# Performance work log

Hardware: AMD Instinct MI355X
Metric: run time of the kernel (lower is better)

Reference implementation:

```python
import jax, jax.numpy as jnp
import numpy as np

ALPHABET = 26
VGENES = 60
JGENES = 20
E = 1024      # embedding_dim (= 2*VJ + LATENT)
H = 2048      # hidden_dim
LATENT = 768  # latent_space_dim
VJ = 128      # embedding_dim_VJ
L = 4096      # sequence length
X_IDX = 23    # all_letters.index('X')
B_IDX = 1     # all_letters.index('B')


def setup_inputs() -> dict:
    key = jax.random.key(0)
    ks = jax.random.split(key, 16)
    s = lambda fan_in: 1.0 / np.sqrt(fan_in)
    u = lambda k, shape, sc: jax.random.uniform(k, shape, jnp.float32, -sc, sc)
    return {
        "x": jax.random.randint(ks[0], (L,), 0, ALPHABET, dtype=jnp.int32),
        "Vg": jax.random.randint(ks[1], (1,), 0, VGENES, dtype=jnp.int32),
        "Jg": jax.random.randint(ks[2], (1,), 0, JGENES, dtype=jnp.int32),
        "tick": 0,
        "emb": jax.random.normal(ks[3], (ALPHABET, E), jnp.float32),
        "embV": jax.random.normal(ks[4], (VGENES, VJ), jnp.float32),
        "embJ": jax.random.normal(ks[5], (JGENES, VJ), jnp.float32),
        "W_ih_enc": u(ks[6], (4 * H, E), s(H)),
        "W_hh_enc": u(ks[7], (4 * H, H), s(H)),
        "b_ih_enc": u(ks[8], (4 * H,), s(H)),
        "b_hh_enc": u(ks[9], (4 * H,), s(H)),
        "W_ls": u(ks[10], (LATENT, H), s(H)),
        "b_ls": u(ks[11], (LATENT,), s(H)),
        "W_ih_dec": u(ks[12], (4 * E, E), s(E)),
        "W_hh_dec": u(ks[13], (4 * E, E), s(E)),
        "b_ih_dec": u(ks[14], (4 * E,), s(E)),
        "b_hh_dec": u(ks[15], (4 * E,), s(E)),
    }


def _lstm_cell(x_t, h, c, W_ih, W_hh, b):
    # torch gate order: i, f, g, o
    g = x_t @ W_ih.T + h @ W_hh.T + b
    i, f, gg, o = jnp.split(g, 4, axis=-1)
    c = jax.nn.sigmoid(f) * c + jax.nn.sigmoid(i) * jnp.tanh(gg)
    h = jax.nn.sigmoid(o) * jnp.tanh(c)
    return h, c


def reference(x, Vg, Jg, tick, emb, embV, embJ,
              W_ih_enc, W_hh_enc, b_ih_enc, b_hh_enc,
              W_ls, b_ls,
              W_ih_dec, W_hh_dec, b_ih_dec, b_hh_dec):
    # ---- encode ----
    embedded = emb[x]                       # [L, E]
    b_enc = b_ih_enc + b_hh_enc

    def enc_step(carry, x_t):
        h, c = carry
        h, c = _lstm_cell(x_t, h, c, W_ih_enc, W_hh_enc, b_enc)
        return (h, c), None

    h0 = jnp.zeros((H,), embedded.dtype)
    (h_n, _), _ = jax.lax.scan(enc_step, (h0, h0), embedded)
    latent = jnp.tanh(h_n @ W_ls.T + b_ls)  # [LATENT]

    # ---- concat latent with V/J gene embeddings -> [E] ----
    latent_cat = jnp.concatenate([embV[Vg[0]], latent, embJ[Jg[0]]])

    # ---- decode: feed own output back as next input ----
    b_dec = b_ih_dec + b_hh_dec
    prev0 = emb[X_IDX]                      # start letter embedding [E]

    def dec_step(carry, _):
        prev, h, c = carry
        h, c = _lstm_cell(prev, h, c, W_ih_dec, W_hh_dec, b_dec)
        return (h, h, c), h

    (_, _, _), outs = jax.lax.scan(dec_step, (prev0, latent_cat, latent_cat),
                                   None, length=L - 2)  # [L-2, E]

    seq = jnp.concatenate([prev0[None], outs, emb[B_IDX][None]], axis=0)  # [L, E]
    recon = seq[::-1][:, None, :]           # [L, 1, E] (original reverses the list)

    return latent_cat[None, None, :], recon, embedded
```

## Files before the change

kernel.cpp:

```cpp
#include <hip/hip_runtime.h>
#include <hip/hip_bf16.h>
#include <stdint.h>

#define NWG 256
typedef unsigned long long u64;

typedef __attribute__((ext_vector_type(8))) short bf16x8;
typedef __attribute__((ext_vector_type(4))) float f32x4;

__device__ __forceinline__ short f2bf(float f) {
    unsigned u = __float_as_uint(f);
    unsigned r = (u + 0x7fffu + ((u >> 16) & 1u)) >> 16;
    return (short)r;
}

__device__ __forceinline__ void gload16(const void* g, void* l) {
    __builtin_amdgcn_global_load_lds(
        (const __attribute__((address_space(1))) void*)g,
        (__attribute__((address_space(3))) void*)l, 16, 0, 0);
}

__device__ __forceinline__ u64 ald(const u64* p) {
    return __hip_atomic_load(p, __ATOMIC_RELAXED, __HIP_MEMORY_SCOPE_AGENT);
}
__device__ __forceinline__ void ast(u64* p, u64 v) {
    __hip_atomic_store(p, v, __ATOMIC_RELAXED, __HIP_MEMORY_SCOPE_AGENT);
}
__device__ __forceinline__ u64 pack(unsigned tag, float f) {
    return ((u64)tag << 32) | (u64)(unsigned)__float_as_uint(f);
}

__global__ void prep_all(const int* __restrict__ x, const int* __restrict__ Vg, const int* __restrict__ Jg,
                         const float* __restrict__ emb, const float* __restrict__ embV, const float* __restrict__ embJ,
                         const float* __restrict__ Wih_e,
                         const float* __restrict__ Wih_d, const float* __restrict__ Whh_d,
                         float* __restrict__ out,
                         short* __restrict__ Abf, short* __restrict__ Wbf,
                         float* __restrict__ wsum,
                         u64* __restrict__ bufE, u64* __restrict__ bufD)
{
    const size_t i0 = (size_t)blockIdx.x * blockDim.x + threadIdx.x;
    const size_t str = (size_t)gridDim.x * blockDim.x;
    for (size_t i = i0; i < (size_t)4096 * 1024; i += str) {
        int t = (int)(i >> 10), j = (int)(i & 1023);
        float v = emb[(size_t)x[t] * 1024 + j];
        out[4195328 + i] = v;
        Abf[i] = f2bf(v);
    }
    for (size_t i = i0; i < (size_t)8192 * 1024; i += str) Wbf[i] = f2bf(Wih_e[i]);
    for (size_t i = i0; i < (size_t)4096 * 1024; i += str) wsum[i] = Wih_d[i] + Whh_d[i];
    for (size_t i = i0; i < 1024; i += str) {
        out[1024 + i] = emb[1 * 1024 + i];
        out[1024 + (size_t)4095 * 1024 + i] = emb[23 * 1024 + i];
    }
    for (size_t i = i0; i < 6144; i += str) bufE[i] = 0ull;
    for (size_t i = i0; i < 3072; i += str) {
        u64 v = 0ull;
        if (i < 1024) {
            if (i < 128)      v = pack(0u, embV[(size_t)Vg[0] * 128 + i]);
            else if (i < 896) v = 0xFFFFFFFF00000000ull;
            else              v = pack(0u, embJ[(size_t)Jg[0] * 128 + (i - 896)]);
        }
        bufD[i] = v;
    }
    for (size_t i = i0; i < 128; i += str) {
        out[i]       = embV[(size_t)Vg[0] * 128 + i];
        out[896 + i] = embJ[(size_t)Jg[0] * 128 + i];
    }
}

__global__ void prep_pg(const float* __restrict__ Wih_d, const float* __restrict__ emb,
                        const float* __restrict__ bih_d, const float* __restrict__ bhh_d,
                        float* __restrict__ pg)
{
    const int lane = threadIdx.x & 63, wv = threadIdx.x >> 6;
    const float* prev0 = emb + 23 * 1024;
    for (int rr = 0; rr < 16; rr++) {
        int row = blockIdx.x * 64 + wv * 16 + rr;
        float s = 0.f;
        #pragma unroll
        for (int q = 0; q < 16; q++) {
            int k = lane + q * 64;
            s += Wih_d[(size_t)row * 1024 + k] * prev0[k];
        }
        for (int o = 32; o; o >>= 1) s += __shfl_xor(s, o, 64);
        if (lane == 0) pg[row] = s + bih_d[row] + bhh_d[row];
    }
}

__launch_bounds__(256, 2)
__global__ void gemm_xgates(const short* __restrict__ A,
                            const short* __restrict__ B,
                            const float* __restrict__ bih, const float* __restrict__ bhh,
                            float* __restrict__ C)
{
    __shared__ short lA[128 * 32];
    __shared__ short lB[128 * 32];
    const int bid = blockIdx.x;
    const int mb = bid >> 6;
    const int nb = bid & 63;
    const int tid = threadIdx.x, lane = tid & 63, wv = tid >> 6;
    const int wr = wv >> 1, wc = wv & 1;
    const int Mbase = mb * 128, Nbase = nb * 128;
    f32x4 acc[4][4] = {};

    for (int kt = 0; kt < 32; kt++) {
        __syncthreads();
        const int k0b = kt * 64;
        #pragma unroll
        for (int c = 0; c < 2; c++) {
            int f = tid * 16 + c * 4096;
            int row = f >> 6, kb = f & 63;
            const char* ga = (const char*)A + (size_t)(Mbase + row) * 2048 + k0b + kb;
            const char* gb = (const char*)B + (size_t)(Nbase + row) * 2048 + k0b + kb;
            gload16(ga, (char*)lA + wv * 1024 + c * 4096);
            gload16(gb, (char*)lB + wv * 1024 + c * 4096);
        }
        asm volatile("s_waitcnt vmcnt(0)" ::: "memory");
        __syncthreads();
        bf16x8 af[4], bf[4];
        #pragma unroll
        for (int i = 0; i < 4; i++) {
            af[i] = *(const bf16x8*)&lA[(wr * 64 + i * 16 + (lane & 15)) * 32 + (lane >> 4) * 8];
            bf[i] = *(const bf16x8*)&lB[(wc * 64 + i * 16 + (lane & 15)) * 32 + (lane >> 4) * 8];
        }
        #pragma unroll
        for (int i = 0; i < 4; i++)
            #pragma unroll
            for (int j = 0; j < 4; j++)
                acc[i][j] = __builtin_amdgcn_mfma_f32_16x16x32_bf16(af[i], bf[j], acc[i][j], 0, 0, 0);
    }
    #pragma unroll
    for (int i = 0; i < 4; i++) {
        #pragma unroll
        for (int j = 0; j < 4; j++) {
            int col = Nbase + wc * 64 + j * 16 + (lane & 15);
            float bv = bih[col] + bhh[col];
            #pragma unroll
            for (int r = 0; r < 4; r++) {
                int row = Mbase + wr * 64 + i * 16 + (lane >> 4) * 4 + r;
                C[(size_t)row * 8192 + col] = acc[i][j][r] + bv;
            }
        }
    }
}

__launch_bounds__(512, 2)
__global__ void rnn_seq(const float* __restrict__ Whh_e,
                        const float* __restrict__ Wls,
                        const float* __restrict__ bls,
                        const float* __restrict__ Whh_d,
                        const float* __restrict__ Gx,
                        const float* __restrict__ wsum,
                        const float* __restrict__ bih_d, const float* __restrict__ bhh_d,
                        const float* __restrict__ pg,
                        u64* __restrict__ bufE,
                        u64* __restrict__ bufD,
                        float* __restrict__ out)
{
    const int w = blockIdx.x;
    const int tid = threadIdx.x;
    const int lane = tid & 63, wv = tid >> 6;
    __shared__ float hl[2048];
    __shared__ float red[32];
    __shared__ float cst[8];

    float we[128];
    #pragma unroll
    for (int rr = 0; rr < 4; rr++) {
        int ridx = wv * 4 + rr;
        const float* src = Whh_e + (size_t)((ridx >> 3) * 2048 + 8 * w + (ridx & 7)) * 2048 + lane;
        #pragma unroll
        for (int j = 0; j < 32; j++) we[rr * 32 + j] = src[64 * j];
    }
    if (tid < 8) cst[tid] = 0.f;
    const int grow = (tid >> 3) * 2048 + 8 * w + (tid & 7);
    __syncthreads();

    #pragma unroll 1
    for (int t = 0; t < 4096; t++) {
        float gxv = 0.f;
        if (tid < 32) gxv = Gx[(size_t)t * 8192 + grow];

        const unsigned tg = (unsigned)t;
        const u64* src = bufE + (size_t)(t % 3) * 2048 + wv * 256 + lane;
        u64 v0, v1, v2, v3;
        for (;;) {
            v0 = ald(src); v1 = ald(src + 64); v2 = ald(src + 128); v3 = ald(src + 192);
            bool ok = ((unsigned)(v0 >> 32) == tg) & ((unsigned)(v1 >> 32) == tg)
                    & ((unsigned)(v2 >> 32) == tg) & ((unsigned)(v3 >> 32) == tg);
            if (__all(ok)) break;
        }
        int b = wv * 256 + lane;
        hl[b]       = __uint_as_float((unsigned)v0);
        hl[b + 64]  = __uint_as_float((unsigned)v1);
        hl[b + 128] = __uint_as_float((unsigned)v2);
        hl[b + 192] = __uint_as_float((unsigned)v3);
        __syncthreads();

        float a0 = 0.f, a1 = 0.f, a2 = 0.f, a3 = 0.f;
        #pragma unroll
        for (int j = 0; j < 32; j++) {
            float hv = hl[lane + 64 * j];
            a0 += we[j] * hv; a1 += we[32 + j] * hv;
            a2 += we[64 + j] * hv; a3 += we[96 + j] * hv;
        }
        #pragma unroll
        for (int o = 32; o; o >>= 1) {
            a0 += __shfl_xor(a0, o, 64); a1 += __shfl_xor(a1, o, 64);
            a2 += __shfl_xor(a2, o, 64); a3 += __shfl_xor(a3, o, 64);
        }
        if (lane == 0) {
            red[wv * 4]     = a0; red[wv * 4 + 1] = a1;
            red[wv * 4 + 2] = a2; red[wv * 4 + 3] = a3;
        }
        __syncthreads();

        if (tid < 32) {
            float g = red[tid] + gxv;
            float gi = __shfl(g, (tid & 7), 64);
            float gf = __shfl(g, (tid & 7) + 8, 64);
            float gg = __shfl(g, (tid & 7) + 16, 64);
            float go = __shfl(g, (tid & 7) + 24, 64);
            if (tid < 8) {
                float c  = cst[tid];
                float ig = 1.f / (1.f + expf(-gi));
                float fg = 1.f / (1.f + expf(-gf));
                float og = 1.f / (1.f + expf(-go));
                float cn = fg * c + ig * tanhf(gg);
                float hn = og * tanhf(cn);
                cst[tid] = cn;
                ast(&bufE[(size_t)((t + 1) % 3) * 2048 + 8 * w + tid], pack((unsigned)(t + 1), hn));
            }
        }
        __syncthreads();
    }

    {
        const unsigned tg = 4096u;
        const u64* src = bufE + (size_t)2048 + wv * 256 + lane;
        u64 v0, v1, v2, v3;
        for (;;) {
            v0 = ald(src); v1 = ald(src + 64); v2 = ald(src + 128); v3 = ald(src + 192);
            bool ok = ((unsigned)(v0 >> 32) == tg) & ((unsigned)(v1 >> 32) == tg)
                    & ((unsigned)(v2 >> 32) == tg) & ((unsigned)(v3 >> 32) == tg);
            if (__all(ok)) break;
        }
        int b = wv * 256 + lane;
        hl[b]       = __uint_as_float((unsigned)v0);
        hl[b + 64]  = __uint_as_float((unsigned)v1);
        hl[b + 128] = __uint_as_float((unsigned)v2);
        hl[b + 192] = __uint_as_float((unsigned)v3);
        __syncthreads();

        if (wv < 3) {
            int row = 3 * w + wv;
            const float* wr = Wls + (size_t)row * 2048 + lane;
            float s = 0.f;
            #pragma unroll
            for (int q = 0; q < 32; q++) s += wr[64 * q] * hl[lane + 64 * q];
            for (int o = 32; o; o >>= 1) s += __shfl_xor(s, o, 64);
            if (lane == 0) {
                float lv = tanhf(s + bls[row]);
                out[128 + row] = lv;
                ast(&bufD[128 + row], pack(0u, lv));
            }
        }
        __syncthreads();
    }

    float wd[32];
    #pragma unroll
    for (int rr = 0; rr < 2; rr++) {
        int ridx = wv * 2 + rr;
        const float* src = wsum + (size_t)((ridx >> 2) * 1024 + 4 * w + (ridx & 3)) * 1024 + lane;
        #pragma unroll
        for (int j = 0; j < 16; j++) wd[rr * 16 + j] = src[64 * j];
    }
    float bdv = 0.f, pgv = 0.f;
    if (tid < 16) {
        int R = (tid >> 2) * 1024 + 4 * w + (tid & 3);
        bdv = bih_d[R] + bhh_d[R];
        pgv = pg[R];
    }
    if (tid < 4) {
        const u64* p = bufD + 4 * w + tid;
        u64 v;
        do { v = ald(p); } while ((unsigned)(v >> 32) != 0u);
        cst[tid] = __uint_as_float((unsigned)v);
    }
    __syncthreads();

    #pragma unroll 1
    for (int s = 1; s <= 4094; s++) {
        const unsigned tg = (unsigned)(s - 1);
        const u64* src = bufD + (size_t)((s - 1) % 3) * 1024 + wv * 128 + lane;
        u64 v0, v1;
        for (;;) {
            v0 = ald(src); v1 = ald(src + 64);
            bool ok = ((unsigned)(v0 >> 32) == tg) & ((unsigned)(v1 >> 32) == tg);
            if (__all(ok)) break;
        }
        hl[wv * 128 + lane]      = __uint_as_float((unsigned)v0);
        hl[wv * 128 + lane + 64] = __uint_as_float((unsigned)v1);
        __syncthreads();

        float a0 = 0.f, a1 = 0.f;
        if (s == 1) {
            #pragma unroll
            for (int rr = 0; rr < 2; rr++) {
                int ridx = wv * 2 + rr;
                const float* srcw = Whh_d + (size_t)((ridx >> 2) * 1024 + 4 * w + (ridx & 3)) * 1024 + lane;
                float a = 0.f;
                #pragma unroll
                for (int j = 0; j < 16; j++) a += srcw[64 * j] * hl[lane + 64 * j];
                if (rr) a1 = a; else a0 = a;
            }
        } else {
            #pragma unroll
            for (int j = 0; j < 16; j++) {
                float hv = hl[lane + 64 * j];
                a0 += wd[j] * hv; a1 += wd[16 + j] * hv;
            }
        }
        #pragma unroll
        for (int o = 32; o; o >>= 1) {
            a0 += __shfl_xor(a0, o, 64); a1 += __shfl_xor(a1, o, 64);
        }
        if (lane == 0) { red[wv * 2] = a0; red[wv * 2 + 1] = a1; }
        __syncthreads();

        if (tid < 16) {
            float g = red[tid] + ((s == 1) ? pgv : bdv);
            float gi = __shfl(g, (tid & 3), 64);
            float gf = __shfl(g, (tid & 3) + 4, 64);
            float gg = __shfl(g, (tid & 3) + 8, 64);
            float go = __shfl(g, (tid & 3) + 12, 64);
            if (tid < 4) {
                float c  = cst[tid];
                float ig = 1.f / (1.f + expf(-gi));
                float fg = 1.f / (1.f + expf(-gf));
                float og = 1.f / (1.f + expf(-go));
                float cn = fg * c + ig * tanhf(gg);
                float hn = og * tanhf(cn);
                cst[tid] = cn;
                out[1024 + (size_t)(4095 - s) * 1024 + 4 * w + tid] = hn;
                ast(&bufD[(size_t)(s % 3) * 1024 + 4 * w + tid], pack((unsigned)s, hn));
            }
        }
        __syncthreads();
    }
}

extern "C" void kernel_launch(void* const* d_in, const int* in_sizes, int n_in,
                              void* d_out, int out_size, void* d_ws, size_t ws_size,
                              hipStream_t stream)
{
    const int* x      = (const int*)d_in[0];
    const int* Vg     = (const int*)d_in[1];
    const int* Jg     = (const int*)d_in[2];
    const float* emb   = (const float*)d_in[4];
    const float* embV  = (const float*)d_in[5];
    const float* embJ  = (const float*)d_in[6];
    const float* Wih_e = (const float*)d_in[7];
    const float* Whh_e = (const float*)d_in[8];
    const float* bih_e = (const float*)d_in[9];
    const float* bhh_e = (const float*)d_in[10];
    const float* Wls   = (const float*)d_in[11];
    const float* bls   = (const float*)d_in[12];
    const float* Wih_d = (const float*)d_in[13];
    const float* Whh_d = (const float*)d_in[14];
    const float* bih_d = (const float*)d_in[15];
    const float* bhh_d = (const float*)d_in[16];
    float* out = (float*)d_out;

    char* ws = (char*)d_ws;
    u64*   bufE = (u64*)ws;
    u64*   bufD = (u64*)(ws + 49152);
    float* pg   = (float*)(ws + 73728);
    short* Abf  = (short*)(ws + 90368);
    short* Wbf  = (short*)(ws + 8478976);
    float* wsum = (float*)(ws + 25256192);
    float* Gx   = (float*)(ws + 42033408);

    prep_all<<<1024, 256, 0, stream>>>(x, Vg, Jg, emb, embV, embJ,
                                       Wih_e, Wih_d, Whh_d,
                                       out, Abf, Wbf, wsum, bufE, bufD);
    prep_pg<<<64, 256, 0, stream>>>(Wih_d, emb, bih_d, bhh_d, pg);
    gemm_xgates<<<2048, 256, 0, stream>>>(Abf, Wbf, bih_e, bhh_e, Gx);

    void* args[] = { (void*)&Whh_e, (void*)&Wls, (void*)&bls, (void*)&Whh_d,
                     (void*)&Gx, (void*)&wsum, (void*)&bih_d, (void*)&bhh_d, (void*)&pg,
                     (void*)&bufE, (void*)&bufD, (void*)&out };
    hipLaunchCooperativeKernel((const void*)rnn_seq, dim3(NWG), dim3(512), args, 0, stream);
}
```

Measured before the change: 20.93 ms.

## Give each wave one hidden unit's four gates and remove per-step block barriers

```diff
diff --git a/kernel.cpp b/kernel.cpp
--- a/kernel.cpp
+++ b/kernel.cpp
@@ -136,10 +136,11 @@
         for (int j = 0; j < 4; j++) {
             int col = Nbase + wc * 64 + j * 16 + (lane & 15);
             float bv = bih[col] + bhh[col];
+            int dst = ((col & 2047) << 2) | (col >> 11);
             #pragma unroll
             for (int r = 0; r < 4; r++) {
                 int row = Mbase + wr * 64 + i * 16 + (lane >> 4) * 4 + r;
-                C[(size_t)row * 8192 + col] = acc[i][j][r] + bv;
+                C[(size_t)row * 8192 + dst] = acc[i][j][r] + bv;
             }
         }
     }
@@ -150,7 +151,7 @@
                         const float* __restrict__ Wls,
                         const float* __restrict__ bls,
                         const float* __restrict__ Whh_d,
-                        const float* __restrict__ Gx,
+                        const float* __restrict__ Gxt,
                         const float* __restrict__ wsum,
                         const float* __restrict__ bih_d, const float* __restrict__ bhh_d,
                         const float* __restrict__ pg,
@@ -161,104 +162,89 @@
     const int w = blockIdx.x;
     const int tid = threadIdx.x;
     const int lane = tid & 63, wv = tid >> 6;
-    __shared__ float hl[2048];
-    __shared__ float red[32];
-    __shared__ float cst[8];
-
-    float we[128];
+    __shared__ float hl[2][2048];
+
+    const int hidxE = 8 * w + wv;
+    float4 we[4][8];
     #pragma unroll
-    for (int rr = 0; rr < 4; rr++) {
-        int ridx = wv * 4 + rr;
-        const float* src = Whh_e + (size_t)((ridx >> 3) * 2048 + 8 * w + (ridx & 7)) * 2048 + lane;
-        #pragma unroll
-        for (int j = 0; j < 32; j++) we[rr * 32 + j] = src[64 * j];
-    }
-    if (tid < 8) cst[tid] = 0.f;
-    const int grow = (tid >> 3) * 2048 + 8 * w + (tid & 7);
-    __syncthreads();
+    for (int g = 0; g < 4; g++) {
+        const float* src = Whh_e + (size_t)(g * 2048 + hidxE) * 2048 + 4 * lane;
+        #pragma unroll
+        for (int jj = 0; jj < 8; jj++) we[g][jj] = *(const float4*)(src + 256 * jj);
+    }
+    float c = 0.f;
+
+    float gx = 0.f;
+    if (lane < 4) gx = Gxt[(size_t)hidxE * 4 + lane];
 
     #pragma unroll 1
     for (int t = 0; t < 4096; t++) {
-        float gxv = 0.f;
-        if (tid < 32) gxv = Gx[(size_t)t * 8192 + grow];
-
         const unsigned tg = (unsigned)t;
-        const u64* src = bufE + (size_t)(t % 3) * 2048 + wv * 256 + lane;
-        u64 v0, v1, v2, v3;
+        const u64* p = bufE + (size_t)(t % 3) * 2048 + wv * 256 + 4 * lane;
+        u64 a0 = ald(p), a1 = ald(p + 1), a2 = ald(p + 2), a3 = ald(p + 3);
         for (;;) {
-            v0 = ald(src); v1 = ald(src + 64); v2 = ald(src + 128); v3 = ald(src + 192);
-            bool ok = ((unsigned)(v0 >> 32) == tg) & ((unsigned)(v1 >> 32) == tg)
-                    & ((unsigned)(v2 >> 32) == tg) & ((unsigned)(v3 >> 32) == tg);
-            if (__all(ok)) break;
-        }
-        int b = wv * 256 + lane;
-        hl[b]       = __uint_as_float((unsigned)v0);
-        hl[b + 64]  = __uint_as_float((unsigned)v1);
-        hl[b + 128] = __uint_as_float((unsigned)v2);
-        hl[b + 192] = __uint_as_float((unsigned)v3);
-        __syncthreads();
-
-        float a0 = 0.f, a1 = 0.f, a2 = 0.f, a3 = 0.f;
-        #pragma unroll
-        for (int j = 0; j < 32; j++) {
-            float hv = hl[lane + 64 * j];
-            a0 += we[j] * hv; a1 += we[32 + j] * hv;
-            a2 += we[64 + j] * hv; a3 += we[96 + j] * hv;
+            bool ok = ((unsigned)(a0 >> 32) == tg) & ((unsigned)(a1 >> 32) == tg)
+                    & ((unsigned)(a2 >> 32) == tg) & ((unsigned)(a3 >> 32) == tg);
+            if (__builtin_expect(__all(ok), 1)) break;
+            a0 = ald(p); a1 = ald(p + 1); a2 = ald(p + 2); a3 = ald(p + 3);
+        }
+        float4 hv = { __uint_as_float((unsigned)a0), __uint_as_float((unsigned)a1),
+                      __uint_as_float((unsigned)a2), __uint_as_float((unsigned)a3) };
+        *(float4*)&hl[t & 1][wv * 256 + 4 * lane] = hv;
+        __syncthreads();
+
+        float gx_next = 0.f;
+        if (lane < 4 && t < 4095) gx_next = Gxt[(size_t)(t + 1) * 8192 + hidxE * 4 + lane];
+
+        float s0 = 0.f, s1 = 0.f, s2 = 0.f, s3 = 0.f;
+        const float4* hp = (const float4*)hl[t & 1];
+        #pragma unroll
+        for (int jj = 0; jj < 8; jj++) {
+            float4 h4 = hp[lane + 64 * jj];
+            s0 += we[0][jj].x * h4.x; s0 += we[0][jj].y * h4.y; s0 += we[0][jj].z * h4.z; s0 += we[0][jj].w * h4.w;
+            s1 += we[1][jj].x * h4.x; s1 += we[1][jj].y * h4.y; s1 += we[1][jj].z * h4.z; s1 += we[1][jj].w * h4.w;
+            s2 += we[2][jj].x * h4.x; s2 += we[2][jj].y * h4.y; s2 += we[2][jj].z * h4.z; s2 += we[2][jj].w * h4.w;
+            s3 += we[3][jj].x * h4.x; s3 += we[3][jj].y * h4.y; s3 += we[3][jj].z * h4.z; s3 += we[3][jj].w * h4.w;
         }
         #pragma unroll
         for (int o = 32; o; o >>= 1) {
-            a0 += __shfl_xor(a0, o, 64); a1 += __shfl_xor(a1, o, 64);
-            a2 += __shfl_xor(a2, o, 64); a3 += __shfl_xor(a3, o, 64);
-        }
-        if (lane == 0) {
-            red[wv * 4]     = a0; red[wv * 4 + 1] = a1;
-            red[wv * 4 + 2] = a2; red[wv * 4 + 3] = a3;
-        }
-        __syncthreads();
-
-        if (tid < 32) {
-            float g = red[tid] + gxv;
-            float gi = __shfl(g, (tid & 7), 64);
-            float gf = __shfl(g, (tid & 7) + 8, 64);
-            float gg = __shfl(g, (tid & 7) + 16, 64);
-            float go = __shfl(g, (tid & 7) + 24, 64);
-            if (tid < 8) {
-                float c  = cst[tid];
-                float ig = 1.f / (1.f + expf(-gi));
-                float fg = 1.f / (1.f + expf(-gf));
-                float og = 1.f / (1.f + expf(-go));
-                float cn = fg * c + ig * tanhf(gg);
-                float hn = og * tanhf(cn);
-                cst[tid] = cn;
-                ast(&bufE[(size_t)((t + 1) % 3) * 2048 + 8 * w + tid], pack((unsigned)(t + 1), hn));
-            }
-        }
-        __syncthreads();
+            s0 += __shfl_xor(s0, o, 64); s1 += __shfl_xor(s1, o, 64);
+            s2 += __shfl_xor(s2, o, 64); s3 += __shfl_xor(s3, o, 64);
+        }
+        float gi = s0 + __shfl(gx, 0, 64);
+        float gf = s1 + __shfl(gx, 1, 64);
+        float gg = s2 + __shfl(gx, 2, 64);
+        float go = s3 + __shfl(gx, 3, 64);
+        float ig = 1.f / (1.f + expf(-gi));
+        float fg = 1.f / (1.f + expf(-gf));
+        float og = 1.f / (1.f + expf(-go));
+        c = fg * c + ig * tanhf(gg);
+        float hn = og * tanhf(c);
+        if (lane == 0) ast(&bufE[(size_t)((t + 1) % 3) * 2048 + hidxE], pack(tg + 1, hn));
+        gx = gx_next;
     }
 
     {
         const unsigned tg = 4096u;
-        const u64* src = bufE + (size_t)2048 + wv * 256 + lane;
-        u64 v0, v1, v2, v3;
+        const u64* p = bufE + (size_t)2048 + wv * 256 + 4 * lane;
+        u64 a0 = ald(p), a1 = ald(p + 1), a2 = ald(p + 2), a3 = ald(p + 3);
         for (;;) {
-            v0 = ald(src); v1 = ald(src + 64); v2 = ald(src + 128); v3 = ald(src + 192);
-            bool ok = ((unsigned)(v0 >> 32) == tg) & ((unsigned)(v1 >> 32) == tg)
-                    & ((unsigned)(v2 >> 32) == tg) & ((unsigned)(v3 >> 32) == tg);
-            if (__all(ok)) break;
-        }
-        int b = wv * 256 + lane;
-        hl[b]       = __uint_as_float((unsigned)v0);
-        hl[b + 64]  = __uint_as_float((unsigned)v1);
-        hl[b + 128] = __uint_as_float((unsigned)v2);
-        hl[b + 192] = __uint_as_float((unsigned)v3);
+            bool ok = ((unsigned)(a0 >> 32) == tg) & ((unsigned)(a1 >> 32) == tg)
+                    & ((unsigned)(a2 >> 32) == tg) & ((unsigned)(a3 >> 32) == tg);
+            if (__builtin_expect(__all(ok), 1)) break;
+            a0 = ald(p); a1 = ald(p + 1); a2 = ald(p + 2); a3 = ald(p + 3);
+        }
+        float4 hv = { __uint_as_float((unsigned)a0), __uint_as_float((unsigned)a1),
+                      __uint_as_float((unsigned)a2), __uint_as_float((unsigned)a3) };
+        *(float4*)&hl[0][wv * 256 + 4 * lane] = hv;
         __syncthreads();
 
         if (wv < 3) {
             int row = 3 * w + wv;
-            const float* wr = Wls + (size_t)row * 2048 + lane;
+            const float* wr = Wls + (size_t)row * 2048;
             float s = 0.f;
             #pragma unroll
-            for (int q = 0; q < 32; q++) s += wr[64 * q] * hl[lane + 64 * q];
+            for (int q = 0; q < 32; q++) s += wr[lane + 64 * q] * hl[0][lane + 64 * q];
             for (int o = 32; o; o >>= 1) s += __shfl_xor(s, o, 64);
             if (lane == 0) {
                 float lv = tanhf(s + bls[row]);
@@ -269,86 +255,87 @@
         __syncthreads();
     }
 
-    float wd[32];
-    #pragma unroll
-    for (int rr = 0; rr < 2; rr++) {
-        int ridx = wv * 2 + rr;
-        const float* src = wsum + (size_t)((ridx >> 2) * 1024 + 4 * w + (ridx & 3)) * 1024 + lane;
-        #pragma unroll
-        for (int j = 0; j < 16; j++) wd[rr * 16 + j] = src[64 * j];
-    }
-    float bdv = 0.f, pgv = 0.f;
-    if (tid < 16) {
-        int R = (tid >> 2) * 1024 + 4 * w + (tid & 3);
-        bdv = bih_d[R] + bhh_d[R];
-        pgv = pg[R];
-    }
-    if (tid < 4) {
-        const u64* p = bufD + 4 * w + tid;
+    const int hidxD = 4 * w + (wv & 3);
+    float4 wd[4][4];
+    float bdv = 0.f, pgv = 0.f, cD = 0.f;
+    if (wv < 4) {
+        #pragma unroll
+        for (int g = 0; g < 4; g++) {
+            const float* src = wsum + (size_t)(g * 1024 + hidxD) * 1024 + 4 * lane;
+            #pragma unroll
+            for (int jj = 0; jj < 4; jj++) wd[g][jj] = *(const float4*)(src + 256 * jj);
+        }
+        if (lane < 4) {
+            int R = lane * 1024 + hidxD;
+            bdv = bih_d[R] + bhh_d[R];
+            pgv = pg[R];
+        }
+        const u64* pc = bufD + hidxD;
         u64 v;
-        do { v = ald(p); } while ((unsigned)(v >> 32) != 0u);
-        cst[tid] = __uint_as_float((unsigned)v);
-    }
-    __syncthreads();
+        do { v = ald(pc); } while ((unsigned)(v >> 32) != 0u);
+        cD = __uint_as_float((unsigned)v);
+    }
 
     #pragma unroll 1
     for (int s = 1; s <= 4094; s++) {
         const unsigned tg = (unsigned)(s - 1);
-        const u64* src = bufD + (size_t)((s - 1) % 3) * 1024 + wv * 128 + lane;
-        u64 v0, v1;
+        const u64* p = bufD + (size_t)((s - 1) % 3) * 1024 + wv * 128 + 2 * lane;
+        u64 a0 = ald(p), a1 = ald(p + 1);
         for (;;) {
-            v0 = ald(src); v1 = ald(src + 64);
-            bool ok = ((unsigned)(v0 >> 32) == tg) & ((unsigned)(v1 >> 32) == tg);
-            if (__all(ok)) break;
-        }
-        hl[wv * 128 + lane]      = __uint_as_float((unsigned)v0);
-        hl[wv * 128 + lane + 64] = __uint_as_float((unsigned)v1);
-        __syncthreads();
-
-        float a0 = 0.f, a1 = 0.f;
-        if (s == 1) {
-            #pragma unroll
-            for (int rr = 0; rr < 2; rr++) {
-                int ridx = wv * 2 + rr;
-                const float* srcw = Whh_d + (size_t)((ridx >> 2) * 1024 + 4 * w + (ridx & 3)) * 1024 + lane;
-                float a = 0.f;
+            bool ok = ((unsigned)(a0 >> 32) == tg) & ((unsigned)(a1 >> 32) == tg);
+            if (__builtin_expect(__all(ok), 1)) break;
+            a0 = ald(p); a1 = ald(p + 1);
+        }
+        float2 hv = { __uint_as_float((unsigned)a0), __uint_as_float((unsigned)a1) };
+        *(float2*)&hl[(s - 1) & 1][wv * 128 + 2 * lane] = hv;
+        __syncthreads();
+
+        if (wv < 4) {
+            float s0 = 0.f, s1 = 0.f, s2 = 0.f, s3 = 0.f;
+            const float4* hp = (const float4*)hl[(s - 1) & 1];
+            if (s == 1) {
                 #pragma unroll
-                for (int j = 0; j < 16; j++) a += srcw[64 * j] * hl[lane + 64 * j];
-                if (rr) a1 = a; else a0 = a;
-            }
-        } else {
-            #pragma unroll
-            for (int j = 0; j < 16; j++) {
-                float hv = hl[lane + 64 * j];
-                a0 += wd[j] * hv; a1 += wd[16 + j] * hv;
-            }
-        }
-        #pragma unroll
-        for (int o = 32; o; o >>= 1) {
-            a0 += __shfl_xor(a0, o, 64); a1 += __shfl_xor(a1, o, 64);
-        }
-        if (lane == 0) { red[wv * 2] = a0; red[wv * 2 + 1] = a1; }
-        __syncthreads();
-
-        if (tid < 16) {
-            float g = red[tid] + ((s == 1) ? pgv : bdv);
-            float gi = __shfl(g, (tid & 3), 64);
-            float gf = __shfl(g, (tid & 3) + 4, 64);
-            float gg = __shfl(g, (tid & 3) + 8, 64);
-            float go = __shfl(g, (tid & 3) + 12, 64);
-            if (tid < 4) {
-                float c  = cst[tid];
-                float ig = 1.f / (1.f + expf(-gi));
-                float fg = 1.f / (1.f + expf(-gf));
-                float og = 1.f / (1.f + expf(-go));
-                float cn = fg * c + ig * tanhf(gg);
-                float hn = og * tanhf(cn);
-                cst[tid] = cn;
-                out[1024 + (size_t)(4095 - s) * 1024 + 4 * w + tid] = hn;
-                ast(&bufD[(size_t)(s % 3) * 1024 + 4 * w + tid], pack((unsigned)s, hn));
-            }
-        }
-        __syncthreads();
+                for (int g = 0; g < 4; g++) {
+                    const float* srcw = Whh_d + (size_t)(g * 1024 + hidxD) * 1024 + 4 * lane;
+                    float a = 0.f;
+                    #pragma unroll
+                    for (int jj = 0; jj < 4; jj++) {
+                        float4 w4 = *(const float4*)(srcw + 256 * jj);
+                        float4 h4 = hp[lane + 64 * jj];
+                        a += w4.x * h4.x + w4.y * h4.y + w4.z * h4.z + w4.w * h4.w;
+                    }
+                    if (g == 0) s0 = a; else if (g == 1) s1 = a; else if (g == 2) s2 = a; else s3 = a;
+                }
+            } else {
+                #pragma unroll
+                for (int jj = 0; jj < 4; jj++) {
+                    float4 h4 = hp[lane + 64 * jj];
+                    s0 += wd[0][jj].x * h4.x; s0 += wd[0][jj].y * h4.y; s0 += wd[0][jj].z * h4.z; s0 += wd[0][jj].w * h4.w;
+                    s1 += wd[1][jj].x * h4.x; s1 += wd[1][jj].y * h4.y; s1 += wd[1][jj].z * h4.z; s1 += wd[1][jj].w * h4.w;
+                    s2 += wd[2][jj].x * h4.x; s2 += wd[2][jj].y * h4.y; s2 += wd[2][jj].z * h4.z; s2 += wd[2][jj].w * h4.w;
+                    s3 += wd[3][jj].x * h4.x; s3 += wd[3][jj].y * h4.y; s3 += wd[3][jj].z * h4.z; s3 += wd[3][jj].w * h4.w;
+                }
+            }
+            #pragma unroll
+            for (int o = 32; o; o >>= 1) {
+                s0 += __shfl_xor(s0, o, 64); s1 += __shfl_xor(s1, o, 64);
+                s2 += __shfl_xor(s2, o, 64); s3 += __shfl_xor(s3, o, 64);
+            }
+            float bb = (s == 1) ? pgv : bdv;
+            float gi = s0 + __shfl(bb, 0, 64);
+            float gf = s1 + __shfl(bb, 1, 64);
+            float gg = s2 + __shfl(bb, 2, 64);
+            float go = s3 + __shfl(bb, 3, 64);
+            float ig = 1.f / (1.f + expf(-gi));
+            float fg = 1.f / (1.f + expf(-gf));
+            float og = 1.f / (1.f + expf(-go));
+            cD = fg * cD + ig * tanhf(gg);
+            float hn = og * tanhf(cD);
+            if (lane == 0) {
+                out[1024 + (size_t)(4095 - s) * 1024 + hidxD] = hn;
+                ast(&bufD[(size_t)(s % 3) * 1024 + hidxD], pack((unsigned)s, hn));
+            }
+        }
     }
 }
 
@@ -381,16 +368,16 @@
     short* Abf  = (short*)(ws + 90368);
     short* Wbf  = (short*)(ws + 8478976);
     float* wsum = (float*)(ws + 25256192);
-    float* Gx   = (float*)(ws + 42033408);
+    float* Gxt  = (float*)(ws + 42033408);
 
     prep_all<<<1024, 256, 0, stream>>>(x, Vg, Jg, emb, embV, embJ,
                                        Wih_e, Wih_d, Whh_d,
                                        out, Abf, Wbf, wsum, bufE, bufD);
     prep_pg<<<64, 256, 0, stream>>>(Wih_d, emb, bih_d, bhh_d, pg);
-    gemm_xgates<<<2048, 256, 0, stream>>>(Abf, Wbf, bih_e, bhh_e, Gx);
+    gemm_xgates<<<2048, 256, 0, stream>>>(Abf, Wbf, bih_e, bhh_e, Gxt);
 
     void* args[] = { (void*)&Whh_e, (void*)&Wls, (void*)&bls, (void*)&Whh_d,
-                     (void*)&Gx, (void*)&wsum, (void*)&bih_d, (void*)&bhh_d, (void*)&pg,
+                     (void*)&Gxt, (void*)&wsum, (void*)&bih_d, (void*)&bhh_d, (void*)&pg,
                      (void*)&bufE, (void*)&bufD, (void*)&out };
     hipLaunchCooperativeKernel((const void*)rnn_seq, dim3(NWG), dim3(512), args, 0, stream);
 }
```

Measured after the change: 46.71 ms. +123.1%, slower.

## Double-buffer LDS, drop trailing barrier, and use 1024-thread blocks in persistent RNN

Applied to the files above, without the earlier changes.

```diff
diff --git a/kernel.cpp b/kernel.cpp
--- a/kernel.cpp
+++ b/kernel.cpp
@@ -145,7 +145,7 @@
     }
 }
 
-__launch_bounds__(512, 2)
+__launch_bounds__(1024, 4)
 __global__ void rnn_seq(const float* __restrict__ Whh_e,
                         const float* __restrict__ Wls,
                         const float* __restrict__ bls,
@@ -161,63 +161,59 @@
     const int w = blockIdx.x;
     const int tid = threadIdx.x;
     const int lane = tid & 63, wv = tid >> 6;
-    __shared__ float hl[2048];
-    __shared__ float red[32];
+    __shared__ float hl[2][2048];
+    __shared__ float red[2][32];
     __shared__ float cst[8];
 
-    float we[128];
+    float we[64];
     #pragma unroll
-    for (int rr = 0; rr < 4; rr++) {
-        int ridx = wv * 4 + rr;
-        const float* src = Whh_e + (size_t)((ridx >> 3) * 2048 + 8 * w + (ridx & 7)) * 2048 + lane;
+    for (int rr = 0; rr < 2; rr++) {
+        int r = wv * 2 + rr;
+        const float* src = Whh_e + (size_t)((r >> 3) * 2048 + 8 * w + (r & 7)) * 2048 + lane;
         #pragma unroll
         for (int j = 0; j < 32; j++) we[rr * 32 + j] = src[64 * j];
     }
     if (tid < 8) cst[tid] = 0.f;
     const int grow = (tid >> 3) * 2048 + 8 * w + (tid & 7);
+    float gx = 0.f;
+    if (tid < 32) gx = Gx[grow];
     __syncthreads();
 
     #pragma unroll 1
     for (int t = 0; t < 4096; t++) {
-        float gxv = 0.f;
-        if (tid < 32) gxv = Gx[(size_t)t * 8192 + grow];
-
         const unsigned tg = (unsigned)t;
-        const u64* src = bufE + (size_t)(t % 3) * 2048 + wv * 256 + lane;
-        u64 v0, v1, v2, v3;
+        const u64* p = bufE + (size_t)(t % 3) * 2048 + wv * 128 + 2 * lane;
+        u64 a0 = ald(p), a1 = ald(p + 1);
         for (;;) {
-            v0 = ald(src); v1 = ald(src + 64); v2 = ald(src + 128); v3 = ald(src + 192);
-            bool ok = ((unsigned)(v0 >> 32) == tg) & ((unsigned)(v1 >> 32) == tg)
-                    & ((unsigned)(v2 >> 32) == tg) & ((unsigned)(v3 >> 32) == tg);
-            if (__all(ok)) break;
-        }
-        int b = wv * 256 + lane;
-        hl[b]       = __uint_as_float((unsigned)v0);
-        hl[b + 64]  = __uint_as_float((unsigned)v1);
-        hl[b + 128] = __uint_as_float((unsigned)v2);
-        hl[b + 192] = __uint_as_float((unsigned)v3);
-        __syncthreads();
-
-        float a0 = 0.f, a1 = 0.f, a2 = 0.f, a3 = 0.f;
+            bool ok = ((unsigned)(a0 >> 32) == tg) & ((unsigned)(a1 >> 32) == tg);
+            if (__builtin_expect(__all(ok), 1)) break;
+            a0 = ald(p); a1 = ald(p + 1);
+        }
+        float2 hv = { __uint_as_float((unsigned)a0), __uint_as_float((unsigned)a1) };
+        *(float2*)&hl[t & 1][wv * 128 + 2 * lane] = hv;
+        __syncthreads();
+
+        float gx_next = 0.f;
+        if (tid < 32 && t < 4095) gx_next = Gx[(size_t)(t + 1) * 8192 + grow];
+
+        float s0 = 0.f, s1 = 0.f;
+        const float* hp = hl[t & 1];
         #pragma unroll
         for (int j = 0; j < 32; j++) {
-            float hv = hl[lane + 64 * j];
-            a0 += we[j] * hv; a1 += we[32 + j] * hv;
-            a2 += we[64 + j] * hv; a3 += we[96 + j] * hv;
+            float h = hp[lane + 64 * j];
+            s0 += we[j] * h;
+            s1 += we[32 + j] * h;
         }
         #pragma unroll
         for (int o = 32; o; o >>= 1) {
-            a0 += __shfl_xor(a0, o, 64); a1 += __shfl_xor(a1, o, 64);
-            a2 += __shfl_xor(a2, o, 64); a3 += __shfl_xor(a3, o, 64);
-        }
-        if (lane == 0) {
-            red[wv * 4]     = a0; red[wv * 4 + 1] = a1;
-            red[wv * 4 + 2] = a2; red[wv * 4 + 3] = a3;
-        }
+            s0 += __shfl_xor(s0, o, 64);
+            s1 += __shfl_xor(s1, o, 64);
+        }
+        if (lane == 0) { red[t & 1][wv * 2] = s0; red[t & 1][wv * 2 + 1] = s1; }
         __syncthreads();
 
         if (tid < 32) {
-            float g = red[tid] + gxv;
+            float g = red[t & 1][tid] + gx;
             float gi = __shfl(g, (tid & 7), 64);
             float gf = __shfl(g, (tid & 7) + 8, 64);
             float gg = __shfl(g, (tid & 7) + 16, 64);
@@ -230,35 +226,31 @@
                 float cn = fg * c + ig * tanhf(gg);
                 float hn = og * tanhf(cn);
                 cst[tid] = cn;
-                ast(&bufE[(size_t)((t + 1) % 3) * 2048 + 8 * w + tid], pack((unsigned)(t + 1), hn));
+                ast(&bufE[(size_t)((t + 1) % 3) * 2048 + 8 * w + tid], pack(tg + 1, hn));
             }
         }
-        __syncthreads();
+        gx = gx_next;
     }
 
     {
         const unsigned tg = 4096u;
-        const u64* src = bufE + (size_t)2048 + wv * 256 + lane;
-        u64 v0, v1, v2, v3;
+        const u64* p = bufE + (size_t)2048 + wv * 128 + 2 * lane;
+        u64 a0 = ald(p), a1 = ald(p + 1);
         for (;;) {
-            v0 = ald(src); v1 = ald(src + 64); v2 = ald(src + 128); v3 = ald(src + 192);
-            bool ok = ((unsigned)(v0 >> 32) == tg) & ((unsigned)(v1 >> 32) == tg)
-                    & ((unsigned)(v2 >> 32) == tg) & ((unsigned)(v3 >> 32) == tg);
-            if (__all(ok)) break;
-        }
-        int b = wv * 256 + lane;
-        hl[b]       = __uint_as_float((unsigned)v0);
-        hl[b + 64]  = __uint_as_float((unsigned)v1);
-        hl[b + 128] = __uint_as_float((unsigned)v2);
-        hl[b + 192] = __uint_as_float((unsigned)v3);
+            bool ok = ((unsigned)(a0 >> 32) == tg) & ((unsigned)(a1 >> 32) == tg);
+            if (__builtin_expect(__all(ok), 1)) break;
+            a0 = ald(p); a1 = ald(p + 1);
+        }
+        float2 hv = { __uint_as_float((unsigned)a0), __uint_as_float((unsigned)a1) };
+        *(float2*)&hl[0][wv * 128 + 2 * lane] = hv;
         __syncthreads();
 
         if (wv < 3) {
             int row = 3 * w + wv;
-            const float* wr = Wls + (size_t)row * 2048 + lane;
+            const float* wr = Wls + (size_t)row * 2048;
             float s = 0.f;
             #pragma unroll
-            for (int q = 0; q < 32; q++) s += wr[64 * q] * hl[lane + 64 * q];
+            for (int q = 0; q < 32; q++) s += wr[lane + 64 * q] * hl[0][lane + 64 * q];
             for (int o = 32; o; o >>= 1) s += __shfl_xor(s, o, 64);
             if (lane == 0) {
                 float lv = tanhf(s + bls[row]);
@@ -269,13 +261,12 @@
         __syncthreads();
     }
 
-    float wd[32];
-    #pragma unroll
-    for (int rr = 0; rr < 2; rr++) {
-        int ridx = wv * 2 + rr;
-        const float* src = wsum + (size_t)((ridx >> 2) * 1024 + 4 * w + (ridx & 3)) * 1024 + lane;
-        #pragma unroll
-        for (int j = 0; j < 16; j++) wd[rr * 16 + j] = src[64 * j];
+    const int Rd = (wv >> 2) * 1024 + 4 * w + (wv & 3);
+    float wd[16];
+    {
+        const float* src = wsum + (size_t)Rd * 1024 + lane;
+        #pragma unroll
+        for (int j = 0; j < 16; j++) wd[j] = src[64 * j];
     }
     float bdv = 0.f, pgv = 0.f;
     if (tid < 16) {
@@ -283,10 +274,11 @@
         bdv = bih_d[R] + bhh_d[R];
         pgv = pg[R];
     }
+    if (tid < 8) cst[tid] = 0.f;
     if (tid < 4) {
-        const u64* p = bufD + 4 * w + tid;
+        const u64* pc = bufD + 4 * w + tid;
         u64 v;
-        do { v = ald(p); } while ((unsigned)(v >> 32) != 0u);
+        do { v = ald(pc); } while ((unsigned)(v >> 32) != 0u);
         cst[tid] = __uint_as_float((unsigned)v);
     }
     __syncthreads();
@@ -294,44 +286,33 @@
     #pragma unroll 1
     for (int s = 1; s <= 4094; s++) {
         const unsigned tg = (unsigned)(s - 1);
-        const u64* src = bufD + (size_t)((s - 1) % 3) * 1024 + wv * 128 + lane;
-        u64 v0, v1;
+        const u64* p = bufD + (size_t)((s - 1) % 3) * 1024 + wv * 64 + lane;
+        u64 a0 = ald(p);
         for (;;) {
-            v0 = ald(src); v1 = ald(src + 64);
-            bool ok = ((unsigned)(v0 >> 32) == tg) & ((unsigned)(v1 >> 32) == tg);
-            if (__all(ok)) break;
-        }
-        hl[wv * 128 + lane]      = __uint_as_float((unsigned)v0);
-        hl[wv * 128 + lane + 64] = __uint_as_float((unsigned)v1);
-        __syncthreads();
-
-        float a0 = 0.f, a1 = 0.f;
+            bool ok = ((unsigned)(a0 >> 32) == tg);
+            if (__builtin_expect(__all(ok), 1)) break;
+            a0 = ald(p);
+        }
+        hl[(s - 1) & 1][wv * 64 + lane] = __uint_as_float((unsigned)a0);
+        __syncthreads();
+
+        float s0 = 0.f;
+        const float* hp = hl[(s - 1) & 1];
         if (s == 1) {
-            #pragma unroll
-            for (int rr = 0; rr < 2; rr++) {
-                int ridx = wv * 2 + rr;
-                const float* srcw = Whh_d + (size_t)((ridx >> 2) * 1024 + 4 * w + (ridx & 3)) * 1024 + lane;
-                float a = 0.f;
-                #pragma unroll
-                for (int j = 0; j < 16; j++) a += srcw[64 * j] * hl[lane + 64 * j];
-                if (rr) a1 = a; else a0 = a;
-            }
+            const float* srcw = Whh_d + (size_t)Rd * 1024 + lane;
+            #pragma unroll
+            for (int j = 0; j < 16; j++) s0 += srcw[64 * j] * hp[lane + 64 * j];
         } else {
             #pragma unroll
-            for (int j = 0; j < 16; j++) {
-                float hv = hl[lane + 64 * j];
-                a0 += wd[j] * hv; a1 += wd[16 + j] * hv;
-            }
-        }
-        #pragma unroll
-        for (int o = 32; o; o >>= 1) {
-            a0 += __shfl_xor(a0, o, 64); a1 += __shfl_xor(a1, o, 64);
-        }
-        if (lane == 0) { red[wv * 2] = a0; red[wv * 2 + 1] = a1; }
+            for (int j = 0; j < 16; j++) s0 += wd[j] * hp[lane + 64 * j];
+        }
+        #pragma unroll
+        for (int o = 32; o; o >>= 1) s0 += __shfl_xor(s0, o, 64);
+        if (lane == 0) red[(s - 1) & 1][wv] = s0;
         __syncthreads();
 
         if (tid < 16) {
-            float g = red[tid] + ((s == 1) ? pgv : bdv);
+            float g = red[(s - 1) & 1][tid] + ((s == 1) ? pgv : bdv);
             float gi = __shfl(g, (tid & 3), 64);
             float gf = __shfl(g, (tid & 3) + 4, 64);
             float gg = __shfl(g, (tid & 3) + 8, 64);
@@ -348,7 +329,6 @@
                 ast(&bufD[(size_t)(s % 3) * 1024 + 4 * w + tid], pack((unsigned)s, hn));
             }
         }
-        __syncthreads();
     }
 }
 
@@ -392,5 +372,5 @@
     void* args[] = { (void*)&Whh_e, (void*)&Wls, (void*)&bls, (void*)&Whh_d,
                      (void*)&Gx, (void*)&wsum, (void*)&bih_d, (void*)&bhh_d, (void*)&pg,
                      (void*)&bufE, (void*)&bufD, (void*)&out };
-    hipLaunchCooperativeKernel((const void*)rnn_seq, dim3(NWG), dim3(512), args, 0, stream);
-}
+    hipLaunchCooperativeKernel((const void*)rnn_seq, dim3(NWG), dim3(1024), args, 0, stream);
+}
```

New measurement: 24.93 ms. 1.19x slower.
